# Performance work log

Measured on AMD Instinct MI355X. Metric: run time of the kernel, lower is better.

The kernel has to match this reference:

```python
import jax, jax.numpy as jnp
import numpy as np

B, T, D = 4, 4096, 4096
N_EXPERTS = 64
TOP_K = 2


def setup_inputs() -> dict:
    key = jax.random.key(0)
    kx, kw = jax.random.split(key)
    x = jax.random.normal(kx, (B, T, D), dtype=jnp.float32)
    gate_w = jax.random.normal(kw, (N_EXPERTS, D), dtype=jnp.float32) * 0.01
    return {"x": x, "gate_w": gate_w}


def reference(x, gate_w):
    # logits: (B, T, E) = x @ gate_w.T  (Linear, no bias; jitter_noise=0 / eval)
    logits = jnp.einsum("btd,ed->bte", x, gate_w)
    probs = jax.nn.softmax(logits, axis=-1)                 # (B, T, E)
    top_k_vals, top_k_idx = jax.lax.top_k(probs, TOP_K)     # (B, T, K)

    n_tokens = B * T
    idx_flat = top_k_idx.reshape(-1)                        # (N*K,)
    counts = jax.ops.segment_sum(
        jnp.ones_like(idx_flat, dtype=probs.dtype), idx_flat,
        num_segments=N_EXPERTS)                             # (E,)
    f_i = counts / (n_tokens * TOP_K)
    p_i = probs.reshape(n_tokens, N_EXPERTS).mean(axis=0)
    router_loss = N_EXPERTS * jnp.mean(f_i * p_i)
    return top_k_vals, top_k_idx, router_loss
```

## Files before the change

kernel.cpp:

```cpp
#include <hip/hip_runtime.h>
#include <math.h>

#define NE 64
#define NTOK 16384
#define DD 4096
#define TOPK 2
#define BLOCK 512
#define TOKPB 64
#define NSTEP (DD / 32)
#define LGSTR 68

using half8 = __attribute__((ext_vector_type(8))) _Float16;
using f32x4 = __attribute__((ext_vector_type(4))) float;

__device__ __forceinline__ void split8(const f32x4 a, const f32x4 b,
                                       half8& hi, half8& lo) {
#pragma unroll
  for (int i = 0; i < 4; ++i) {
    const float v = a[i] * 64.0f;
    const _Float16 h = (_Float16)v;
    hi[i] = h;
    lo[i] = (_Float16)(v - (float)h);
  }
#pragma unroll
  for (int i = 0; i < 4; ++i) {
    const float v = b[i] * 64.0f;
    const _Float16 h = (_Float16)v;
    hi[4 + i] = h;
    lo[4 + i] = (_Float16)(v - (float)h);
  }
}

__global__ __launch_bounds__(BLOCK) void router_kernel(
    const float* __restrict__ x, const float* __restrict__ gw,
    float* __restrict__ out, float* __restrict__ ws) {
  __shared__ __align__(16) float pl[TOKPB * LGSTR];

  const int tid = threadIdx.x;
  const int lane = tid & 63;
  const int wid = __builtin_amdgcn_readfirstlane(tid >> 6);
  const int mi = wid & 3;
  const int np = wid >> 2;
  const int tok0 = blockIdx.x * TOKPB;
  const int r = lane & 15;
  const int kg = (lane >> 4) * 8;

  const float* xp = x + (size_t)(tok0 + mi * 16 + r) * DD + kg;
  const float* b0p = gw + (size_t)(np * 32 + r) * DD + kg;
  const float* b1p = b0p + (size_t)16 * DD;

  f32x4 acc0 = {0.f, 0.f, 0.f, 0.f};
  f32x4 acc1 = {0.f, 0.f, 0.f, 0.f};

  f32x4 xa0 = *(const f32x4*)(xp + 0);
  f32x4 xb0 = *(const f32x4*)(xp + 4);
  f32x4 xa1 = *(const f32x4*)(xp + 32);
  f32x4 xb1 = *(const f32x4*)(xp + 36);
  f32x4 b0a = *(const f32x4*)(b0p + 0);
  f32x4 b0b = *(const f32x4*)(b0p + 4);
  f32x4 b1a = *(const f32x4*)(b1p + 0);
  f32x4 b1b = *(const f32x4*)(b1p + 4);

#pragma unroll 1
  for (int cc = 0; cc < NSTEP; ++cc) {
    half8 Ah, Al, B0h, B0l, B1h, B1l;
    split8(xa0, xb0, Ah, Al);
    split8(b0a, b0b, B0h, B0l);
    split8(b1a, b1b, B1h, B1l);
    xa0 = xa1;
    xb0 = xb1;
    if (cc + 2 < NSTEP) {
      const int ko = (cc + 2) * 32;
      xa1 = *(const f32x4*)(xp + ko);
      xb1 = *(const f32x4*)(xp + ko + 4);
    }
    if (cc + 1 < NSTEP) {
      const int ko = (cc + 1) * 32;
      b0a = *(const f32x4*)(b0p + ko);
      b0b = *(const f32x4*)(b0p + ko + 4);
      b1a = *(const f32x4*)(b1p + ko);
      b1b = *(const f32x4*)(b1p + ko + 4);
    }
    acc0 = __builtin_amdgcn_mfma_f32_16x16x32_f16(Al, B0h, acc0, 0, 0, 0);
    acc0 = __builtin_amdgcn_mfma_f32_16x16x32_f16(Ah, B0l, acc0, 0, 0, 0);
    acc0 = __builtin_amdgcn_mfma_f32_16x16x32_f16(Ah, B0h, acc0, 0, 0, 0);
    acc1 = __builtin_amdgcn_mfma_f32_16x16x32_f16(Al, B1h, acc1, 0, 0, 0);
    acc1 = __builtin_amdgcn_mfma_f32_16x16x32_f16(Ah, B1l, acc1, 0, 0, 0);
    acc1 = __builtin_amdgcn_mfma_f32_16x16x32_f16(Ah, B1h, acc1, 0, 0, 0);
  }

  {
    const int trow = (lane >> 4) * 4;
#pragma unroll
    for (int i = 0; i < 4; ++i) {
      pl[(mi * 16 + trow + i) * LGSTR + np * 32 + r] =
          acc0[i] * 2.44140625e-4f;
      pl[(mi * 16 + trow + i) * LGSTR + np * 32 + 16 + r] =
          acc1[i] * 2.44140625e-4f;
    }
  }
  __syncthreads();

  float psum_local = 0.f, cnt_local = 0.f;
  float* out_v = out;
  float* out_i = out + NTOK * TOPK;
#pragma unroll 1
  for (int ii = 0; ii < 8; ++ii) {
    const int t = wid * 8 + ii;
    float v = pl[t * LGSTR + lane];
    float m = v;
#pragma unroll
    for (int sh = 32; sh > 0; sh >>= 1) m = fmaxf(m, __shfl_xor(m, sh, 64));
    float ex = expf(v - m);
    float ssum = ex;
#pragma unroll
    for (int sh = 32; sh > 0; sh >>= 1) ssum += __shfl_xor(ssum, sh, 64);
    float p = ex / ssum;
    psum_local += p;

    float v1 = p; int i1 = lane;
#pragma unroll
    for (int sh = 32; sh > 0; sh >>= 1) {
      float ov = __shfl_xor(v1, sh, 64);
      int oi = __shfl_xor(i1, sh, 64);
      if (ov > v1 || (ov == v1 && oi < i1)) { v1 = ov; i1 = oi; }
    }
    float v2 = (lane == i1) ? -INFINITY : p; int i2 = lane;
#pragma unroll
    for (int sh = 32; sh > 0; sh >>= 1) {
      float ov = __shfl_xor(v2, sh, 64);
      int oi = __shfl_xor(i2, sh, 64);
      if (ov > v2 || (ov == v2 && oi < i2)) { v2 = ov; i2 = oi; }
    }
    cnt_local += (lane == i1 ? 1.f : 0.f) + (lane == i2 ? 1.f : 0.f);
    if (lane == 0) {
      const int tg = tok0 + t;
      out_v[tg * 2 + 0] = v1;
      out_v[tg * 2 + 1] = v2;
      out_i[tg * 2 + 0] = (float)i1;
      out_i[tg * 2 + 1] = (float)i2;
    }
  }
  atomicAdd(ws + lane, cnt_local);
  atomicAdd(ws + NE + lane, psum_local);
}

__global__ void loss_kernel(const float* __restrict__ ws,
                            float* __restrict__ out) {
  const int lane = threadIdx.x & 63;
  float f = ws[lane] * (1.f / (float)(NTOK * TOPK));
  float p = ws[NE + lane] * (1.f / (float)NTOK);
  float v = f * p;
#pragma unroll
  for (int sh = 32; sh > 0; sh >>= 1) v += __shfl_xor(v, sh, 64);
  if (lane == 0) out[NTOK * TOPK * 2] = v;
}

extern "C" void kernel_launch(void* const* d_in, const int* in_sizes, int n_in,
                              void* d_out, int out_size, void* d_ws,
                              size_t ws_size, hipStream_t stream) {
  const float* x = (const float*)d_in[0];
  const float* gw = (const float*)d_in[1];
  float* out = (float*)d_out;
  float* ws = (float*)d_ws;

  hipMemsetAsync(d_ws, 0, 2 * NE * sizeof(float), stream);
  router_kernel<<<NTOK / TOKPB, BLOCK, 0, stream>>>(x, gw, out, ws);
  loss_kernel<<<1, 64, 0, stream>>>(ws, out);
}
```

Measured before the change: 239.4 us.

## Presplit gate weights into fp16 hi/lo once and deepen load pipelining

Adds a pre-pass kernel that splits the fp32 gate weights into fp16 high and low halves in workspace, so the router kernel loads ready-made half8 operands instead of re-splitting the weights in every block. The main loop is unrolled by four, with a four-deep register prefetch for x and a two-deep one for the weights. This removes redundant VALU conversion work per block. In exchange it adds an extra launch, needs about 1 MB of workspace (it falls back to the old path otherwise), and raises register pressure.

Result: no change. 241.9 us (+1.0%).

```diff
diff --git a/kernel.cpp b/kernel.cpp
--- a/kernel.cpp
+++ b/kernel.cpp
@@ -10,6 +10,10 @@
 #define NSTEP (DD / 32)
 #define LGSTR 68
 
+#define WSH_OFF 512
+#define WSL_OFF (WSH_OFF + NE * DD * 2)
+#define WS_NEED (WSL_OFF + NE * DD * 2)
+
 using half8 = __attribute__((ext_vector_type(8))) _Float16;
 using f32x4 = __attribute__((ext_vector_type(4))) float;
 
@@ -31,8 +35,22 @@
   }
 }
 
+__global__ void wsplit_kernel(const float* __restrict__ gw,
+                              _Float16* __restrict__ gh,
+                              _Float16* __restrict__ gl) {
+  const int i = (blockIdx.x * 256 + threadIdx.x) * 8;
+  const f32x4 a = *(const f32x4*)(gw + i);
+  const f32x4 b = *(const f32x4*)(gw + i + 4);
+  half8 h, l;
+  split8(a, b, h, l);
+  *(half8*)(gh + i) = h;
+  *(half8*)(gl + i) = l;
+}
+
+template <bool PRE>
 __global__ __launch_bounds__(BLOCK) void router_kernel(
     const float* __restrict__ x, const float* __restrict__ gw,
+    const _Float16* __restrict__ gwh, const _Float16* __restrict__ gwl,
     float* __restrict__ out, float* __restrict__ ws) {
   __shared__ __align__(16) float pl[TOKPB * LGSTR];
 
@@ -46,48 +64,91 @@
   const int kg = (lane >> 4) * 8;
 
   const float* xp = x + (size_t)(tok0 + mi * 16 + r) * DD + kg;
+  const _Float16* bh0 = gwh + (size_t)(np * 32 + r) * DD + kg;
+  const _Float16* bh1 = bh0 + (size_t)16 * DD;
+  const _Float16* bl0 = gwl + (size_t)(np * 32 + r) * DD + kg;
+  const _Float16* bl1 = bl0 + (size_t)16 * DD;
   const float* b0p = gw + (size_t)(np * 32 + r) * DD + kg;
   const float* b1p = b0p + (size_t)16 * DD;
 
   f32x4 acc0 = {0.f, 0.f, 0.f, 0.f};
   f32x4 acc1 = {0.f, 0.f, 0.f, 0.f};
 
-  f32x4 xa0 = *(const f32x4*)(xp + 0);
-  f32x4 xb0 = *(const f32x4*)(xp + 4);
-  f32x4 xa1 = *(const f32x4*)(xp + 32);
-  f32x4 xb1 = *(const f32x4*)(xp + 36);
-  f32x4 b0a = *(const f32x4*)(b0p + 0);
-  f32x4 b0b = *(const f32x4*)(b0p + 4);
-  f32x4 b1a = *(const f32x4*)(b1p + 0);
-  f32x4 b1b = *(const f32x4*)(b1p + 4);
+  f32x4 xa[4], xb[4];
+#pragma unroll
+  for (int j = 0; j < 4; ++j) {
+    xa[j] = *(const f32x4*)(xp + j * 32);
+    xb[j] = *(const f32x4*)(xp + j * 32 + 4);
+  }
+  half8 B0h[2], B0l[2], B1h[2], B1l[2];
+  f32x4 rb0a[2], rb0b[2], rb1a[2], rb1b[2];
+#pragma unroll
+  for (int j = 0; j < 2; ++j) {
+    if constexpr (PRE) {
+      B0h[j] = *(const half8*)(bh0 + j * 32);
+      B0l[j] = *(const half8*)(bl0 + j * 32);
+      B1h[j] = *(const half8*)(bh1 + j * 32);
+      B1l[j] = *(const half8*)(bl1 + j * 32);
+    } else {
+      rb0a[j] = *(const f32x4*)(b0p + j * 32);
+      rb0b[j] = *(const f32x4*)(b0p + j * 32 + 4);
+      rb1a[j] = *(const f32x4*)(b1p + j * 32);
+      rb1b[j] = *(const f32x4*)(b1p + j * 32 + 4);
+    }
+  }
+
+#define SUBSTEP(ST, J, XRELOAD, BRELOAD)                                    \
+  do {                                                                      \
+    half8 Ah, Al;                                                           \
+    split8(xa[J], xb[J], Ah, Al);                                           \
+    if (XRELOAD) {                      \
+      xa[J] = *(const f32x4*)(xp + (ST + 4) * 32);                          \
+      xb[J] = *(const f32x4*)(xp + (ST + 4) * 32 + 4);                      \
+    }                                                                       \
+    half8 h0, l0, h1, l1;                                                   \
+    if constexpr (PRE) {                                                    \
+      h0 = B0h[(J) & 1]; l0 = B0l[(J) & 1];                                 \
+      h1 = B1h[(J) & 1]; l1 = B1l[(J) & 1];                                 \
+      if (BRELOAD) {                                                        \
+        B0h[(J) & 1] = *(const half8*)(bh0 + (ST + 2) * 32);                \
+        B0l[(J) & 1] = *(const half8*)(bl0 + (ST + 2) * 32);                \
+        B1h[(J) & 1] = *(const half8*)(bh1 + (ST + 2) * 32);                \
+        B1l[(J) & 1] = *(const half8*)(bl1 + (ST + 2) * 32);                \
+      }                                                                     \
+    } else {                                                                \
+      split8(rb0a[(J) & 1], rb0b[(J) & 1], h0, l0);                         \
+      split8(rb1a[(J) & 1], rb1b[(J) & 1], h1, l1);                         \
+      if (BRELOAD) {                                                        \
+        rb0a[(J) & 1] = *(const f32x4*)(b0p + (ST + 2) * 32);               \
+        rb0b[(J) & 1] = *(const f32x4*)(b0p + (ST + 2) * 32 + 4);           \
+        rb1a[(J) & 1] = *(const f32x4*)(b1p + (ST + 2) * 32);               \
+        rb1b[(J) & 1] = *(const f32x4*)(b1p + (ST + 2) * 32 + 4);           \
+      }                                                                     \
+    }                                                                       \
+    acc0 = __builtin_amdgcn_mfma_f32_16x16x32_f16(Al, h0, acc0, 0, 0, 0);   \
+    acc0 = __builtin_amdgcn_mfma_f32_16x16x32_f16(Ah, l0, acc0, 0, 0, 0);   \
+    acc0 = __builtin_amdgcn_mfma_f32_16x16x32_f16(Ah, h0, acc0, 0, 0, 0);   \
+    acc1 = __builtin_amdgcn_mfma_f32_16x16x32_f16(Al, h1, acc1, 0, 0, 0);   \
+    acc1 = __builtin_amdgcn_mfma_f32_16x16x32_f16(Ah, l1, acc1, 0, 0, 0);   \
+    acc1 = __builtin_amdgcn_mfma_f32_16x16x32_f16(Ah, h1, acc1, 0, 0, 0);   \
+  } while (0)
 
 #pragma unroll 1
-  for (int cc = 0; cc < NSTEP; ++cc) {
-    half8 Ah, Al, B0h, B0l, B1h, B1l;
-    split8(xa0, xb0, Ah, Al);
-    split8(b0a, b0b, B0h, B0l);
-    split8(b1a, b1b, B1h, B1l);
-    xa0 = xa1;
-    xb0 = xb1;
-    if (cc + 2 < NSTEP) {
-      const int ko = (cc + 2) * 32;
-      xa1 = *(const f32x4*)(xp + ko);
-      xb1 = *(const f32x4*)(xp + ko + 4);
-    }
-    if (cc + 1 < NSTEP) {
-      const int ko = (cc + 1) * 32;
-      b0a = *(const f32x4*)(b0p + ko);
-      b0b = *(const f32x4*)(b0p + ko + 4);
-      b1a = *(const f32x4*)(b1p + ko);
-      b1b = *(const f32x4*)(b1p + ko + 4);
-    }
-    acc0 = __builtin_amdgcn_mfma_f32_16x16x32_f16(Al, B0h, acc0, 0, 0, 0);
-    acc0 = __builtin_amdgcn_mfma_f32_16x16x32_f16(Ah, B0l, acc0, 0, 0, 0);
-    acc0 = __builtin_amdgcn_mfma_f32_16x16x32_f16(Ah, B0h, acc0, 0, 0, 0);
-    acc1 = __builtin_amdgcn_mfma_f32_16x16x32_f16(Al, B1h, acc1, 0, 0, 0);
-    acc1 = __builtin_amdgcn_mfma_f32_16x16x32_f16(Ah, B1l, acc1, 0, 0, 0);
-    acc1 = __builtin_amdgcn_mfma_f32_16x16x32_f16(Ah, B1h, acc1, 0, 0, 0);
-  }
+  for (int i = 0; i < NSTEP / 4 - 1; ++i) {
+    const int st = i * 4;
+    SUBSTEP(st + 0, 0, 1, 1);
+    SUBSTEP(st + 1, 1, 1, 1);
+    SUBSTEP(st + 2, 2, 1, 1);
+    SUBSTEP(st + 3, 3, 1, 1);
+  }
+  {
+    const int st = NSTEP - 4;
+    SUBSTEP(st + 0, 0, 0, 1);
+    SUBSTEP(st + 1, 1, 0, 1);
+    SUBSTEP(st + 2, 2, 0, 0);
+    SUBSTEP(st + 3, 3, 0, 0);
+  }
+#undef SUBSTEP
 
   {
     const int trow = (lane >> 4) * 4;
@@ -164,7 +225,16 @@
   float* out = (float*)d_out;
   float* ws = (float*)d_ws;
 
-  hipMemsetAsync(d_ws, 0, 2 * NE * sizeof(float), stream);
-  router_kernel<<<NTOK / TOKPB, BLOCK, 0, stream>>>(x, gw, out, ws);
+  hipMemsetAsync(d_ws, 0, 512, stream);
+  if (ws_size >= (size_t)WS_NEED) {
+    _Float16* gh = (_Float16*)((char*)d_ws + WSH_OFF);
+    _Float16* gl = (_Float16*)((char*)d_ws + WSL_OFF);
+    wsplit_kernel<<<NE * DD / (256 * 8), 256, 0, stream>>>(gw, gh, gl);
+    router_kernel<true><<<NTOK / TOKPB, BLOCK, 0, stream>>>(x, gw, gh, gl,
+                                                            out, ws);
+  } else {
+    router_kernel<false><<<NTOK / TOKPB, BLOCK, 0, stream>>>(
+        x, gw, nullptr, nullptr, out, ws);
+  }
   loss_kernel<<<1, 64, 0, stream>>>(ws, out);
 }
```
